# Performance work log

Hardware: AMD Instinct MI355X
Metric: run time of the kernel (lower is better)

## Reference

```python
import jax, jax.numpy as jnp
import numpy as np

D_MODEL = 1024
NUM_HEADS = 16
DEPTH = D_MODEL // NUM_HEADS
B, S = 2, 2048


def setup_inputs() -> dict:
    key = jax.random.key(0)
    ks = jax.random.split(key, 13)
    sc = 1.0 / np.sqrt(D_MODEL)
    inp = {
        "q": jax.random.normal(ks[0], (B, S, D_MODEL), jnp.float32),
        "k": jax.random.normal(ks[1], (B, S, D_MODEL), jnp.float32),
        "v": jax.random.normal(ks[2], (B, S, D_MODEL), jnp.float32),
        "mask": jax.random.randint(ks[3], (B, 1, S, S), 0, 2).astype(jnp.float32),
        "wq": jax.random.normal(ks[4], (D_MODEL, D_MODEL), jnp.float32) * sc,
        "bq": jnp.zeros((D_MODEL,), jnp.float32),
        "wk": jax.random.normal(ks[5], (D_MODEL, D_MODEL), jnp.float32) * sc,
        "bk": jnp.zeros((D_MODEL,), jnp.float32),
        "wv": jax.random.normal(ks[6], (D_MODEL, D_MODEL), jnp.float32) * sc,
        "bv": jnp.zeros((D_MODEL,), jnp.float32),
        "wo": jax.random.normal(ks[7], (D_MODEL, D_MODEL), jnp.float32) * sc,
        "bo": jnp.zeros((D_MODEL,), jnp.float32),
    }
    return inp


def _split_heads(x):
    # [B,S,D] -> [B,H,S,depth]
    b, s, _ = x.shape
    return x.reshape(b, s, NUM_HEADS, DEPTH).transpose(0, 2, 1, 3)


def reference(q, k, v, mask, wq, bq, wk, bk, wv, bv, wo, bo):
    qh = _split_heads(q @ wq.T + bq)
    kh = _split_heads(k @ wk.T + bk)
    vh = _split_heads(v @ wv.T + bv)
    logits = jnp.einsum("bhqd,bhkd->bhqk", qh, kh) / jnp.sqrt(
        jnp.asarray(DEPTH, jnp.float32))
    logits = logits + mask * (-1e9)
    attn = jax.nn.softmax(logits, axis=-1)
    out = jnp.einsum("bhqk,bhkd->bhqd", attn, vh)
    out = out.transpose(0, 2, 1, 3).reshape(q.shape[0], -1, D_MODEL)
    return out @ wo.T + bo
```

## Files before the change

kernel.cpp:

```cpp
#include <hip/hip_runtime.h>

#define D_MODEL 1024
#define NHEADS  16
#define DEPTH   64
#define BATCH   2
#define SEQ     2048
#define MROWS   (BATCH * SEQ)
#define QSCALE  0.18033688011112042f

typedef unsigned short u16;
typedef unsigned int   u32;
typedef unsigned long long u64;
typedef __bf16 bf16x8 __attribute__((ext_vector_type(8)));
typedef float  f32x4  __attribute__((ext_vector_type(4)));

#if __has_builtin(__builtin_amdgcn_exp2f)
#define EXP2(x) __builtin_amdgcn_exp2f(x)
#else
#define EXP2(x) exp2f(x)
#endif

__device__ __forceinline__ u16 f2b(float f) {
    return __builtin_bit_cast(u16, static_cast<__bf16>(f));
}
__device__ __forceinline__ bf16x8 ldb8(const u16* p) {
    return __builtin_bit_cast(bf16x8, *(const uint4*)p);
}

__global__ __launch_bounds__(256) void pack_mask(
    const float* __restrict__ mask, u64* __restrict__ bits)
{
    const int w    = blockIdx.x * 4 + (threadIdx.x >> 6);
    const int lane = threadIdx.x & 63;
    float m = mask[(size_t)w * 64 + lane];
    u64 b = __ballot(m > 0.5f);
    if (lane == 0) bits[w] = b;
}

__global__ __launch_bounds__(256, 3) void proj3(
    const float* __restrict__ q, const float* __restrict__ k, const float* __restrict__ v,
    const float* __restrict__ wq, const float* __restrict__ wk, const float* __restrict__ wv,
    const float* __restrict__ bq, const float* __restrict__ bk, const float* __restrict__ bv,
    u16* __restrict__ qws, u16* __restrict__ kws, u16* __restrict__ vtws)
{
    __shared__ __align__(16) u16 ldsA[128 * 40];
    __shared__ __align__(16) u16 ldsB[128 * 40];

    const int z = blockIdx.z;
    const float* X  = (z == 0) ? q  : (z == 1) ? k  : v;
    const float* W  = (z == 0) ? wq : (z == 1) ? wk : wv;
    const float* Bi = (z == 0) ? bq : (z == 1) ? bk : bv;
    u16* dst        = (z == 0) ? qws : (z == 1) ? kws : vtws;

    const int tid  = threadIdx.x;
    const int wv_  = tid >> 6;
    const int lane = tid & 63;
    const int quad = lane >> 4;
    const int l15  = lane & 15;
    const int bx = blockIdx.y >> 2;
    const int by = (blockIdx.x << 2) | (blockIdx.y & 3);
    const int wm = (wv_ >> 1) * 64;
    const int wn = (wv_ & 1) * 64;

    f32x4 acc[4][4];
    for (int i = 0; i < 4; ++i)
        for (int j = 0; j < 4; ++j)
            acc[i][j] = (f32x4){0.f, 0.f, 0.f, 0.f};

    const int rowA0 = by * 128;
    const int rowB0 = bx * 128;

    const int sr = tid >> 3;
    const int sc = (tid & 7) * 4;

    float4 pa[4], pb[4];
    #pragma unroll
    for (int i = 0; i < 4; ++i) {
        pa[i] = *(const float4*)&X[(size_t)(rowA0 + sr + i * 32) * D_MODEL + sc];
        pb[i] = *(const float4*)&W[(size_t)(rowB0 + sr + i * 32) * D_MODEL + sc];
    }

    for (int it = 0; it < 32; ++it) {
        #pragma unroll
        for (int i = 0; i < 4; ++i) {
            ushort4 ha, hb;
            ha.x = f2b(pa[i].x); ha.y = f2b(pa[i].y); ha.z = f2b(pa[i].z); ha.w = f2b(pa[i].w);
            hb.x = f2b(pb[i].x); hb.y = f2b(pb[i].y); hb.z = f2b(pb[i].z); hb.w = f2b(pb[i].w);
            *(ushort4*)&ldsA[(sr + i * 32) * 40 + sc] = ha;
            *(ushort4*)&ldsB[(sr + i * 32) * 40 + sc] = hb;
        }
        __syncthreads();

        if (it < 31) {
            const int k0 = (it + 1) * 32;
            #pragma unroll
            for (int i = 0; i < 4; ++i) {
                pa[i] = *(const float4*)&X[(size_t)(rowA0 + sr + i * 32) * D_MODEL + k0 + sc];
                pb[i] = *(const float4*)&W[(size_t)(rowB0 + sr + i * 32) * D_MODEL + k0 + sc];
            }
        }

        bf16x8 af[4], bfr[4];
        #pragma unroll
        for (int t = 0; t < 4; ++t) {
            af[t]  = ldb8(&ldsA[(wm + t * 16 + l15) * 40 + quad * 8]);
            bfr[t] = ldb8(&ldsB[(wn + t * 16 + l15) * 40 + quad * 8]);
        }
        #pragma unroll
        for (int mt = 0; mt < 4; ++mt)
            #pragma unroll
            for (int nt = 0; nt < 4; ++nt)
                acc[mt][nt] = __builtin_amdgcn_mfma_f32_16x16x32_bf16(af[mt], bfr[nt], acc[mt][nt], 0, 0, 0);
        __syncthreads();
    }

    #pragma unroll
    for (int nt = 0; nt < 4; ++nt) {
        int n = bx * 128 + wn + nt * 16 + l15;
        float bvv = Bi[n];
        int h = n >> 6, d = n & 63;
        #pragma unroll
        for (int mt = 0; mt < 4; ++mt) {
            #pragma unroll
            for (int r = 0; r < 4; ++r) {
                int m = by * 128 + wm + mt * 16 + quad * 4 + r;
                float c = acc[mt][nt][r] + bvv;
                if (z == 0) c *= QSCALE;
                int b = m >> 11, s = m & (SEQ - 1);
                if (z != 2)
                    dst[(((size_t)(b * NHEADS + h) * SEQ) + s) * DEPTH + d] = f2b(c);
                else
                    dst[(((size_t)(b * NHEADS + h) * DEPTH) + d) * SEQ + s] = f2b(c);
            }
        }
    }
}

__global__ __launch_bounds__(256) void gemm_out(
    const u16* __restrict__ X, const float* __restrict__ W,
    const float* __restrict__ bias, float* __restrict__ out)
{
    __shared__ __align__(16) u16 ldsA[128 * 40];
    __shared__ __align__(16) u16 ldsB[64 * 40];

    const int tid  = threadIdx.x;
    const int wv_  = tid >> 6;
    const int lane = tid & 63;
    const int quad = lane >> 4;
    const int l15  = lane & 15;
    const int bx = ((blockIdx.y >> 2) << 1) | (blockIdx.x >> 3);
    const int by = ((blockIdx.x & 7) << 2) | (blockIdx.y & 3);
    const int wm = (wv_ >> 1) * 64;
    const int wn = (wv_ & 1) * 32;

    f32x4 acc[4][2];
    for (int i = 0; i < 4; ++i)
        for (int j = 0; j < 2; ++j)
            acc[i][j] = (f32x4){0.f, 0.f, 0.f, 0.f};

    const int rowA0 = by * 128;
    const int rowB0 = bx * 64;

    const int ar = tid >> 2, akc = (tid & 3) * 8;
    const int br = tid >> 3, bc = (tid & 7) * 4;

    uint4  paA[2];
    float4 paB[2];
    #pragma unroll
    for (int i = 0; i < 2; ++i) {
        paA[i] = *(const uint4*)&X[(size_t)(rowA0 + ar + i * 64) * D_MODEL + akc];
        paB[i] = *(const float4*)&W[(size_t)(rowB0 + br + i * 32) * D_MODEL + bc];
    }

    for (int it = 0; it < 32; ++it) {
        #pragma unroll
        for (int i = 0; i < 2; ++i) {
            *(uint4*)&ldsA[(ar + i * 64) * 40 + akc] = paA[i];
            ushort4 hb;
            hb.x = f2b(paB[i].x); hb.y = f2b(paB[i].y); hb.z = f2b(paB[i].z); hb.w = f2b(paB[i].w);
            *(ushort4*)&ldsB[(br + i * 32) * 40 + bc] = hb;
        }
        __syncthreads();

        if (it < 31) {
            const int k0 = (it + 1) * 32;
            #pragma unroll
            for (int i = 0; i < 2; ++i) {
                paA[i] = *(const uint4*)&X[(size_t)(rowA0 + ar + i * 64) * D_MODEL + k0 + akc];
                paB[i] = *(const float4*)&W[(size_t)(rowB0 + br + i * 32) * D_MODEL + k0 + bc];
            }
        }

        bf16x8 af[4], bfr[2];
        #pragma unroll
        for (int t = 0; t < 4; ++t)
            af[t] = ldb8(&ldsA[(wm + t * 16 + l15) * 40 + quad * 8]);
        #pragma unroll
        for (int t = 0; t < 2; ++t)
            bfr[t] = ldb8(&ldsB[(wn + t * 16 + l15) * 40 + quad * 8]);
        #pragma unroll
        for (int mt = 0; mt < 4; ++mt)
            #pragma unroll
            for (int nt = 0; nt < 2; ++nt)
                acc[mt][nt] = __builtin_amdgcn_mfma_f32_16x16x32_bf16(af[mt], bfr[nt], acc[mt][nt], 0, 0, 0);
        __syncthreads();
    }

    #pragma unroll
    for (int nt = 0; nt < 2; ++nt) {
        int n = bx * 64 + wn + nt * 16 + l15;
        float bvv = bias[n];
        #pragma unroll
        for (int mt = 0; mt < 4; ++mt) {
            #pragma unroll
            for (int r = 0; r < 4; ++r) {
                int m = by * 128 + wm + mt * 16 + quad * 4 + r;
                out[(size_t)m * D_MODEL + n] = acc[mt][nt][r] + bvv;
            }
        }
    }
}

__global__ __launch_bounds__(256, 4) void flash_attn(
    const u16* __restrict__ Q, const u16* __restrict__ K,
    const u16* __restrict__ Vt, const u64* __restrict__ maskbits,
    u16* __restrict__ O)
{
    __shared__ __align__(16) u16 ldsK[2][64 * 64];
    __shared__ __align__(16) u16 ldsV[2][64 * 64];
    __shared__ __align__(16) u16 ldsP[4][16 * 64];

    const int tid  = threadIdx.x;
    const int wv_  = tid >> 6;
    const int lane = tid & 63;
    const int quad = lane >> 4;
    const int l15  = lane & 15;
    const int bh = ((blockIdx.x & 7) << 2) | (blockIdx.y & 3);
    const int qt = ((blockIdx.y >> 2) << 2) | (blockIdx.x >> 3);
    const int b  = bh >> 4, h = bh & 15;
    const int q0 = qt * 64 + wv_ * 16;

    const u16* Qb = Q  + (size_t)bh * SEQ * DEPTH;
    const u16* Kb = K  + (size_t)bh * SEQ * DEPTH;
    const u16* Vb = Vt + (size_t)bh * DEPTH * SEQ;
    const u64* MB = maskbits + (size_t)b * SEQ * (SEQ / 64);

    const int srow = tid >> 3;
    const int sc8  = tid & 7;
    const int swz  = ((sc8 ^ (srow & 7)) * 8);
    const int kdst0 = srow * 64 + swz;
    const int kdst1 = (srow + 32) * 64 + swz;

    const int xk0 = ((quad ^ (l15 & 7)) * 8);
    const int xk1 = (((4 + quad) ^ (l15 & 7)) * 8);

    bf16x8 aq0 = ldb8(&Qb[(q0 + l15) * DEPTH + quad * 8]);
    bf16x8 aq1 = ldb8(&Qb[(q0 + l15) * DEPTH + 32 + quad * 8]);

    bf16x8 vones;
    #pragma unroll
    for (int i = 0; i < 8; ++i) vones[i] = (__bf16)1.0f;

    f32x4 oa[4];
    for (int i = 0; i < 4; ++i) oa[i] = (f32x4){0.f, 0.f, 0.f, 0.f};
    f32x4 lacc = (f32x4){0.f, 0.f, 0.f, 0.f};

    u16* myP = ldsP[wv_];

    int wp[4][4];
    #pragma unroll
    for (int cc = 0; cc < 4; ++cc)
        #pragma unroll
        for (int r = 0; r < 4; ++r) {
            const int row  = quad * 4 + r;
            const int colg = cc * 2 + (l15 >> 3);
            wp[cc][r] = row * 64 + ((colg ^ (row & 7)) * 8) + (l15 & 7);
        }
    const int rp0 = l15 * 64 + ((quad ^ (l15 & 7)) * 8);
    const int rp1 = l15 * 64 + (((4 + quad) ^ (l15 & 7)) * 8);

    uint4 kreg0 = *(const uint4*)&Kb[(size_t)srow * DEPTH + sc8 * 8];
    uint4 kreg1 = *(const uint4*)&Kb[(size_t)(srow + 32) * DEPTH + sc8 * 8];
    uint4 vreg0 = *(const uint4*)&Vb[(size_t)srow * SEQ + sc8 * 8];
    uint4 vreg1 = *(const uint4*)&Vb[(size_t)(srow + 32) * SEQ + sc8 * 8];

    for (int it = 0; it < 32; ++it) {
        const int buf = it & 1;
        u16* Kl = ldsK[buf];
        u16* Vl = ldsV[buf];

        *(uint4*)&Kl[kdst0] = kreg0;
        *(uint4*)&Kl[kdst1] = kreg1;
        *(uint4*)&Vl[kdst0] = vreg0;
        *(uint4*)&Vl[kdst1] = vreg1;
        __syncthreads();

        if (it < 31) {
            const int kb2 = (it + 1) * 64;
            kreg0 = *(const uint4*)&Kb[(size_t)(kb2 + srow) * DEPTH + sc8 * 8];
            kreg1 = *(const uint4*)&Kb[(size_t)(kb2 + srow + 32) * DEPTH + sc8 * 8];
            vreg0 = *(const uint4*)&Vb[(size_t)srow * SEQ + kb2 + sc8 * 8];
            vreg1 = *(const uint4*)&Vb[(size_t)(srow + 32) * SEQ + kb2 + sc8 * 8];
        }

        u32 tlo[4], thi[4];
        #pragma unroll
        for (int r = 0; r < 4; ++r) {
            u64 t = MB[(size_t)(q0 + quad * 4 + r) * (SEQ / 64) + it] >> l15;
            tlo[r] = (u32)t;
            thi[r] = (u32)(t >> 32);
        }

        #pragma unroll
        for (int cc = 0; cc < 4; ++cc) {
            const int row = cc * 16 + l15;
            bf16x8 bk0 = ldb8(&Kl[row * 64 + xk0]);
            bf16x8 bk1 = ldb8(&Kl[row * 64 + xk1]);
            f32x4 z = (f32x4){0.f, 0.f, 0.f, 0.f};
            z = __builtin_amdgcn_mfma_f32_16x16x32_bf16(aq0, bk0, z, 0, 0, 0);
            z = __builtin_amdgcn_mfma_f32_16x16x32_bf16(aq1, bk1, z, 0, 0, 0);
            #pragma unroll
            for (int r = 0; r < 4; ++r) {
                u32 w   = (cc < 2) ? tlo[r] : thi[r];
                u32 bit = (cc & 1) ? ((w >> 16) & 1u) : (w & 1u);
                float e = EXP2(z[r]);
                float p = bit ? 0.f : e;
                myP[wp[cc][r]] = f2b(p);
            }
        }

        __builtin_amdgcn_wave_barrier();
        __builtin_amdgcn_s_waitcnt(0xc07f);
        __builtin_amdgcn_wave_barrier();
        bf16x8 pa0 = ldb8(&myP[rp0]);
        bf16x8 pa1 = ldb8(&myP[rp1]);

        lacc = __builtin_amdgcn_mfma_f32_16x16x32_bf16(pa0, vones, lacc, 0, 0, 0);
        lacc = __builtin_amdgcn_mfma_f32_16x16x32_bf16(pa1, vones, lacc, 0, 0, 0);

        #pragma unroll
        for (int n = 0; n < 4; ++n) {
            const int row = n * 16 + l15;
            bf16x8 bv0 = ldb8(&Vl[row * 64 + xk0]);
            bf16x8 bv1 = ldb8(&Vl[row * 64 + xk1]);
            oa[n] = __builtin_amdgcn_mfma_f32_16x16x32_bf16(pa0, bv0, oa[n], 0, 0, 0);
            oa[n] = __builtin_amdgcn_mfma_f32_16x16x32_bf16(pa1, bv1, oa[n], 0, 0, 0);
        }
    }

    float inv[4];
    #pragma unroll
    for (int r = 0; r < 4; ++r)
        inv[r] = 1.0f / lacc[r];

    #pragma unroll
    for (int n = 0; n < 4; ++n)
        #pragma unroll
        for (int r = 0; r < 4; ++r) {
            int m = q0 + quad * 4 + r;
            O[((size_t)b * SEQ + m) * D_MODEL + h * DEPTH + n * 16 + l15] =
                f2b(oa[n][r] * inv[r]);
        }
}

extern "C" void kernel_launch(void* const* d_in, const int* in_sizes, int n_in,
                              void* d_out, int out_size, void* d_ws, size_t ws_size,
                              hipStream_t stream) {
    const float* q    = (const float*)d_in[0];
    const float* k    = (const float*)d_in[1];
    const float* v    = (const float*)d_in[2];
    const float* mask = (const float*)d_in[3];
    const float* wq   = (const float*)d_in[4];
    const float* bq   = (const float*)d_in[5];
    const float* wk   = (const float*)d_in[6];
    const float* bk   = (const float*)d_in[7];
    const float* wv   = (const float*)d_in[8];
    const float* bv   = (const float*)d_in[9];
    const float* wo   = (const float*)d_in[10];
    const float* bo   = (const float*)d_in[11];

    u16* base = (u16*)d_ws;
    const size_t seg = (size_t)BATCH * NHEADS * SEQ * DEPTH;
    u16* qws  = base;
    u16* kws  = base + seg;
    u16* vtws = base + 2 * seg;
    u16* ows  = base + 3 * seg;
    u64* mbits = (u64*)(base + 4 * seg);

    dim3 blk(256);
    hipLaunchKernelGGL(pack_mask, dim3(BATCH * SEQ * (SEQ / 64) / 4), blk, 0, stream, mask, mbits);

    dim3 gp(D_MODEL / 128, MROWS / 128, 3);
    hipLaunchKernelGGL(proj3, gp, blk, 0, stream,
                       q, k, v, wq, wk, wv, bq, bk, bv, qws, kws, vtws);

    dim3 ga(SEQ / 64, BATCH * NHEADS);
    hipLaunchKernelGGL(flash_attn, ga, blk, 0, stream, qws, kws, vtws, mbits, ows);

    dim3 go(D_MODEL / 64, MROWS / 128);
    hipLaunchKernelGGL(gemm_out, go, blk, 0, stream, ows, wo, bo, (float*)d_out);
}
```

Baseline: 317.5 us.

## Pre-convert projection inputs to bf16 and stream tiles via global_load_lds

Adds a conversion kernel that casts q/k/v and the three projection weights to bf16 in workspace. A new projection GEMM then double-buffers bf16 tiles straight into LDS with global_load_lds, replacing the fused fp32-load-and-convert path. The aim is to halve the GEMM's global traffic, remove per-tile conversion, and overlap loads with MFMA. In exchange it adds an extra launch plus a full fp32 read and bf16 write pass, and it falls back to the old kernel when the workspace is too small.

```diff
diff --git a/kernel.cpp b/kernel.cpp
--- a/kernel.cpp
+++ b/kernel.cpp
@@ -25,6 +25,11 @@
 }
 __device__ __forceinline__ bf16x8 ldb8(const u16* p) {
     return __builtin_bit_cast(bf16x8, *(const uint4*)p);
+}
+__device__ __forceinline__ void gload16(const u16* g, u16* l) {
+    __builtin_amdgcn_global_load_lds(
+        (const __attribute__((address_space(1))) void*)g,
+        (__attribute__((address_space(3))) void*)l, 16, 0, 0);
 }
 
 __global__ __launch_bounds__(256) void pack_mask(
@@ -37,7 +42,129 @@
     if (lane == 0) bits[w] = b;
 }
 
-__global__ __launch_bounds__(256, 3) void proj3(
+__global__ __launch_bounds__(256) void cvt_bf16(
+    const float* __restrict__ q, const float* __restrict__ k, const float* __restrict__ v,
+    const float* __restrict__ wq, const float* __restrict__ wk, const float* __restrict__ wv,
+    u16* __restrict__ xb, u16* __restrict__ wb)
+{
+    const size_t e = ((size_t)blockIdx.x * 256 + threadIdx.x) * 8;
+    const float* src;
+    u16* dst;
+    size_t off;
+    if (e < 12582912) {
+        const int a = (int)(e >> 22);
+        off = e & 4194303;
+        src = (a == 0) ? q : (a == 1) ? k : v;
+        dst = xb + ((size_t)a << 22) + off;
+    } else {
+        const size_t e2 = e - 12582912;
+        const int a = (int)(e2 >> 20);
+        off = e2 & 1048575;
+        src = (a == 0) ? wq : (a == 1) ? wk : wv;
+        dst = wb + ((size_t)a << 20) + off;
+    }
+    const float4 f0 = *(const float4*)(src + off);
+    const float4 f1 = *(const float4*)(src + off + 4);
+    uint4 o;
+    o.x = (u32)f2b(f0.x) | ((u32)f2b(f0.y) << 16);
+    o.y = (u32)f2b(f0.z) | ((u32)f2b(f0.w) << 16);
+    o.z = (u32)f2b(f1.x) | ((u32)f2b(f1.y) << 16);
+    o.w = (u32)f2b(f1.z) | ((u32)f2b(f1.w) << 16);
+    *(uint4*)dst = o;
+}
+
+__global__ __launch_bounds__(256, 3) void proj3_bf16(
+    const u16* __restrict__ xb, const u16* __restrict__ wb,
+    const float* __restrict__ bq, const float* __restrict__ bk, const float* __restrict__ bv,
+    u16* __restrict__ qws, u16* __restrict__ kws, u16* __restrict__ vtws)
+{
+    __shared__ __align__(16) u16 la[2][128 * 32];
+    __shared__ __align__(16) u16 lb[2][128 * 32];
+
+    const int z = blockIdx.z;
+    const u16* X = xb + ((size_t)z << 22);
+    const u16* W = wb + ((size_t)z << 20);
+    const float* Bi = (z == 0) ? bq : (z == 1) ? bk : bv;
+    u16* dst       = (z == 0) ? qws : (z == 1) ? kws : vtws;
+
+    const int tid  = threadIdx.x;
+    const int wv_  = tid >> 6;
+    const int lane = tid & 63;
+    const int quad = lane >> 4;
+    const int l15  = lane & 15;
+    const int bx = blockIdx.y >> 2;
+    const int by = (blockIdx.x << 2) | (blockIdx.y & 3);
+    const int wm = (wv_ >> 1) * 64;
+    const int wn = (wv_ & 1) * 64;
+
+    f32x4 acc[4][4];
+    for (int i = 0; i < 4; ++i)
+        for (int j = 0; j < 4; ++j)
+            acc[i][j] = (f32x4){0.f, 0.f, 0.f, 0.f};
+
+    const int rowA0 = by * 128;
+    const int rowB0 = bx * 128;
+
+    const int strow = tid >> 2;
+    const int stcol = (tid & 3) * 8;
+    const u16* gA0 = &X[(size_t)(rowA0 + strow) * D_MODEL + stcol];
+    const u16* gA1 = gA0 + (size_t)64 * D_MODEL;
+    const u16* gB0 = &W[(size_t)(rowB0 + strow) * D_MODEL + stcol];
+    const u16* gB1 = gB0 + (size_t)64 * D_MODEL;
+    const int l0 = tid * 8, l1 = 2048 + tid * 8;
+
+    gload16(gA0, &la[0][l0]);
+    gload16(gA1, &la[0][l1]);
+    gload16(gB0, &lb[0][l0]);
+    gload16(gB1, &lb[0][l1]);
+    __syncthreads();
+
+    for (int t = 0; t < 32; ++t) {
+        const int buf = t & 1;
+        if (t < 31) {
+            const int ko = (t + 1) * 32;
+            gload16(gA0 + ko, &la[buf ^ 1][l0]);
+            gload16(gA1 + ko, &la[buf ^ 1][l1]);
+            gload16(gB0 + ko, &lb[buf ^ 1][l0]);
+            gload16(gB1 + ko, &lb[buf ^ 1][l1]);
+        }
+        bf16x8 af[4], bfr[4];
+        #pragma unroll
+        for (int tt = 0; tt < 4; ++tt) {
+            af[tt]  = ldb8(&la[buf][(wm + tt * 16 + l15) * 32 + quad * 8]);
+            bfr[tt] = ldb8(&lb[buf][(wn + tt * 16 + l15) * 32 + quad * 8]);
+        }
+        #pragma unroll
+        for (int mt = 0; mt < 4; ++mt)
+            #pragma unroll
+            for (int nt = 0; nt < 4; ++nt)
+                acc[mt][nt] = __builtin_amdgcn_mfma_f32_16x16x32_bf16(af[mt], bfr[nt], acc[mt][nt], 0, 0, 0);
+        __syncthreads();
+    }
+
+    #pragma unroll
+    for (int nt = 0; nt < 4; ++nt) {
+        int n = bx * 128 + wn + nt * 16 + l15;
+        float bvv = Bi[n];
+        int h = n >> 6, d = n & 63;
+        #pragma unroll
+        for (int mt = 0; mt < 4; ++mt) {
+            #pragma unroll
+            for (int r = 0; r < 4; ++r) {
+                int m = by * 128 + wm + mt * 16 + quad * 4 + r;
+                float c = acc[mt][nt][r] + bvv;
+                if (z == 0) c *= QSCALE;
+                int b = m >> 11, s = m & (SEQ - 1);
+                if (z != 2)
+                    dst[(((size_t)(b * NHEADS + h) * SEQ) + s) * DEPTH + d] = f2b(c);
+                else
+                    dst[(((size_t)(b * NHEADS + h) * DEPTH) + d) * SEQ + s] = f2b(c);
+            }
+        }
+    }
+}
+
+__global__ __launch_bounds__(256, 3) void proj3_fused(
     const float* __restrict__ q, const float* __restrict__ k, const float* __restrict__ v,
     const float* __restrict__ wq, const float* __restrict__ wk, const float* __restrict__ wv,
     const float* __restrict__ bq, const float* __restrict__ bk, const float* __restrict__ bv,
@@ -386,13 +513,23 @@
     u16* vtws = base + 2 * seg;
     u16* ows  = base + 3 * seg;
     u64* mbits = (u64*)(base + 4 * seg);
+    u16* xb   = base + 4 * seg + 524288;
+    u16* wb   = xb + 3 * seg;
+    const size_t need_bytes = (4 * seg + 524288 + 3 * seg + 3u * 1048576) * 2;
 
     dim3 blk(256);
     hipLaunchKernelGGL(pack_mask, dim3(BATCH * SEQ * (SEQ / 64) / 4), blk, 0, stream, mask, mbits);
 
     dim3 gp(D_MODEL / 128, MROWS / 128, 3);
-    hipLaunchKernelGGL(proj3, gp, blk, 0, stream,
-                       q, k, v, wq, wk, wv, bq, bk, bv, qws, kws, vtws);
+    if (ws_size >= need_bytes) {
+        hipLaunchKernelGGL(cvt_bf16, dim3(7680), blk, 0, stream,
+                           q, k, v, wq, wk, wv, xb, wb);
+        hipLaunchKernelGGL(proj3_bf16, gp, blk, 0, stream,
+                           xb, wb, bq, bk, bv, qws, kws, vtws);
+    } else {
+        hipLaunchKernelGGL(proj3_fused, gp, blk, 0, stream,
+                           q, k, v, wq, wk, wv, bq, bk, bv, qws, kws, vtws);
+    }
 
     dim3 ga(SEQ / 64, BATCH * NHEADS);
     hipLaunchKernelGGL(flash_attn, ga, blk, 0, stream, qws, kws, vtws, mbits, ows);
```

Result: faster. 303.9 us (-4.3%).
